# Performance work log

Measured on AMD Instinct MI355X. Metric: run time of the kernel, lower is better.

## Reference

```python
import jax, jax.numpy as jnp
import numpy as np

B = 16384
OBJ_FEAT = 1024
PVF_DIM = 1024
PPF_DIM = 64
HIDDEN = 512
OBJ_NUM = 1001        # param['object_num'] + 1
PRED_NUM = 132


def setup_inputs() -> dict:
    key = jax.random.key(0)
    ks = jax.random.split(key, 16)
    s = 0.02
    return {
        "inp_sf":  jax.random.normal(ks[0], (B, OBJ_FEAT), jnp.float32),
        "inp_of":  jax.random.normal(ks[1], (B, OBJ_FEAT), jnp.float32),
        "inp_ppf": jax.random.normal(ks[2], (B, PPF_DIM), jnp.float32),
        "inp_pvf": jax.random.normal(ks[3], (B, PVF_DIM), jnp.float32),
        "gt_s": jax.random.randint(ks[4], (B,), 0, OBJ_NUM, jnp.int32),
        "gt_o": jax.random.randint(ks[5], (B,), 0, OBJ_NUM, jnp.int32),
        # object_predictor: Linear(OBJ_FEAT, HIDDEN) -> Dropout -> ReLU -> Linear(HIDDEN, OBJ_NUM, bias=False)
        "W_obj1": jax.random.normal(ks[6], (OBJ_FEAT, HIDDEN), jnp.float32) * s,
        "b_obj1": jnp.zeros((HIDDEN,), jnp.float32),
        "W_obj2": jax.random.normal(ks[7], (HIDDEN, OBJ_NUM), jnp.float32) * s,
        # predicate_vis_feat_emb: Linear(PVF_DIM, HIDDEN) -> Dropout -> ReLU
        "W_pvf": jax.random.normal(ks[8], (PVF_DIM, HIDDEN), jnp.float32) * s,
        "b_pvf": jnp.zeros((HIDDEN,), jnp.float32),
        # predicate_feat_emb: Linear(HIDDEN + PPF_DIM, HIDDEN) -> ReLU
        "W_pf": jax.random.normal(ks[9], (HIDDEN + PPF_DIM, HIDDEN), jnp.float32) * s,
        "b_pf": jnp.zeros((HIDDEN,), jnp.float32),
        # predicate_predictor: Linear(HIDDEN, PRED_NUM, bias=False)
        "W_pred": jax.random.normal(ks[10], (HIDDEN, PRED_NUM), jnp.float32) * s,
        # knowledge table (frozen) + learnable scalar factor
        "so2p": jax.random.normal(ks[11], (OBJ_NUM * OBJ_NUM, PRED_NUM), jnp.float32) * s,
        "so2p_factor": jnp.zeros((1,), jnp.float32),
    }


def reference(inp_sf, inp_of, inp_ppf, inp_pvf, gt_s, gt_o,
              W_obj1, b_obj1, W_obj2, W_pvf, b_pvf, W_pf, b_pf, W_pred,
              so2p, so2p_factor):
    def obj_predictor(x):
        h = jnp.maximum(x @ W_obj1 + b_obj1, 0.0)  # Dropout is identity (p=0 / eval)
        return h @ W_obj2

    s_score = obj_predictor(inp_sf)               # [B, OBJ_NUM]
    o_score = obj_predictor(inp_of)               # [B, OBJ_NUM]

    pvf_emb = jnp.maximum(inp_pvf @ W_pvf + b_pvf, 0.0)                     # [B, HIDDEN]
    pf_emb = jnp.maximum(jnp.concatenate([pvf_emb, inp_ppf], axis=1) @ W_pf + b_pf, 0.0)
    p_score = pf_emb @ W_pred                     # [B, PRED_NUM]

    # one-hot(s) (x) one-hot(o) flattened then matmul with so2p == row gather at s*OBJ_NUM + o
    so_bias = so2p[gt_s * OBJ_NUM + gt_o]         # [B, PRED_NUM]
    so_bias = so_bias * jnp.exp(so2p_factor)      # use_knowledge=True

    return (s_score, o_score, p_score + so_bias)
```

## Files before the change

kernel.cpp:

```cpp
#include <hip/hip_runtime.h>
#include <hip/hip_bf16.h>
#include <cstdint>
#include <cstddef>

constexpr int BROWS   = 16384;
constexpr int OBJ_FEAT = 1024;
constexpr int PPF_DIM  = 64;
constexpr int HIDDEN   = 512;
constexpr int OBJ_NUM  = 1001;
constexpr int PRED_NUM = 132;
constexpr int OBJ_PAD  = 1024;
constexpr int PRED_PAD = 256;
constexpr int PF_K     = HIDDEN + PPF_DIM;

typedef __attribute__((ext_vector_type(8))) short bf16x8;
typedef __attribute__((ext_vector_type(4))) float f32x4;

static __device__ __forceinline__ unsigned short f2bf(float f) {
  unsigned int u = __float_as_uint(f);
  u += 0x7fffu + ((u >> 16) & 1u);
  return (unsigned short)(u >> 16);
}

__global__ void cast_w_all(const float* __restrict__ W0, const float* __restrict__ W1,
                           const float* __restrict__ W2, const float* __restrict__ W3,
                           const float* __restrict__ W4,
                           unsigned short* __restrict__ T0, unsigned short* __restrict__ T1,
                           unsigned short* __restrict__ T2, unsigned short* __restrict__ T3,
                           unsigned short* __restrict__ T4) {
  const int z = blockIdx.z;
  const float* W; unsigned short* T; int K, N, Npad;
  if      (z == 0) { W = W0; T = T0; K = 1024; N = 512;  Npad = 512;  }
  else if (z == 1) { W = W1; T = T1; K = 512;  N = 1001; Npad = 1024; }
  else if (z == 2) { W = W2; T = T2; K = 1024; N = 512;  Npad = 512;  }
  else if (z == 3) { W = W3; T = T3; K = 576;  N = 512;  Npad = 512;  }
  else             { W = W4; T = T4; K = 512;  N = 132;  Npad = 256;  }
  int n = blockIdx.y;
  int k = blockIdx.x * 256 + threadIdx.x;
  if (n >= Npad || k >= K) return;
  float v = (n < N) ? W[(size_t)k * N + n] : 0.0f;
  T[(size_t)n * K + k] = f2bf(v);
}

__global__ void cast_act(const float* __restrict__ sf, const float* __restrict__ of,
                         const float* __restrict__ pvf, const float* __restrict__ ppf,
                         unsigned short* __restrict__ Abf, unsigned short* __restrict__ Pvfb,
                         unsigned short* __restrict__ Ppfb) {
  const int z = blockIdx.z;
  const float* src; unsigned short* dst; size_t n4;
  if (z == 0)      { src = sf;  dst = Abf;                          n4 = (size_t)BROWS * OBJ_FEAT / 4; }
  else if (z == 1) { src = of;  dst = Abf + (size_t)BROWS * OBJ_FEAT; n4 = (size_t)BROWS * OBJ_FEAT / 4; }
  else if (z == 2) { src = pvf; dst = Pvfb;                         n4 = (size_t)BROWS * OBJ_FEAT / 4; }
  else             { src = ppf; dst = Ppfb;                         n4 = (size_t)BROWS * PPF_DIM / 4; }
  size_t stride = (size_t)gridDim.x * 256;
  for (size_t i = (size_t)blockIdx.x * 256 + threadIdx.x; i < n4; i += stride) {
    float4 v = reinterpret_cast<const float4*>(src)[i];
    ushort4 o;
    o.x = f2bf(v.x); o.y = f2bf(v.y); o.z = f2bf(v.z); o.w = f2bf(v.w);
    reinterpret_cast<ushort4*>(dst)[i] = o;
  }
}

template <int MODE>
__global__ __launch_bounds__(256)
void gemm_bf16(const unsigned short* __restrict__ A1, int ldA1, int K1,
               const unsigned short* __restrict__ A2, int ldA2,
               const unsigned short* __restrict__ Bt, int K,
               int Msplit,
               const unsigned short* __restrict__ A1b,
               const unsigned short* __restrict__ Btb,
               const float* __restrict__ biasb,
               float* __restrict__ outF, unsigned short* __restrict__ outB,
               int ldout, int Nreal,
               const float* __restrict__ bias,
               const int* __restrict__ gts, const int* __restrict__ gto,
               const float* __restrict__ so2p, const float* __restrict__ factor) {
  __shared__ unsigned short sA[128 * 32];
  __shared__ unsigned short sB[128 * 32];

  const int tid  = threadIdx.x;
  const int lane = tid & 63;
  const int wave = tid >> 6;
  const int wm   = wave >> 1;
  const int wn   = wave & 1;
  const int quad = lane >> 4;
  const int r16  = lane & 15;

  const int nwg = gridDim.x * gridDim.y;
  const int id  = blockIdx.y * gridDim.x + blockIdx.x;
  const int cpx = nwg >> 3;
  const int t   = (id & 7) * cpx + (id >> 3);
  const int m0  = (t / gridDim.x) * 128;
  const int n0  = (t % gridDim.x) * 128;

  const unsigned short* Abase = A1;
  const unsigned short* Bbase = Bt;
  const float* bias_p = bias;
  int mA = m0;
  if (m0 >= Msplit) { Abase = A1b; Bbase = Btb; bias_p = biasb; mA = m0 - Msplit; }

  f32x4 acc[4][4] = {};

  for (int k0 = 0; k0 < K; k0 += 32) {
    __syncthreads();
    const unsigned short* As; int lda, kk;
    if (k0 < K1) { As = Abase; lda = ldA1; kk = k0; }
    else         { As = A2;    lda = ldA2; kk = k0 - K1; }
#pragma unroll
    for (int j = 0; j < 2; ++j) {
      int ch = tid + j * 256, row = ch >> 2, c8 = ch & 3;
      const unsigned short* ga = As + (size_t)(mA + row) * lda + kk + c8 * 8;
      __builtin_amdgcn_global_load_lds(
          (const __attribute__((address_space(1))) void*)ga,
          (__attribute__((address_space(3))) void*)(sA + ch * 8), 16, 0, 0);
      const unsigned short* gb = Bbase + (size_t)(n0 + row) * K + k0 + c8 * 8;
      __builtin_amdgcn_global_load_lds(
          (const __attribute__((address_space(1))) void*)gb,
          (__attribute__((address_space(3))) void*)(sB + ch * 8), 16, 0, 0);
    }
    __syncthreads();

    bf16x8 af[4], bfr[4];
#pragma unroll
    for (int i = 0; i < 4; ++i)
      af[i] = *reinterpret_cast<const bf16x8*>(sA + (wm * 64 + i * 16 + r16) * 32 + quad * 8);
#pragma unroll
    for (int j = 0; j < 4; ++j)
      bfr[j] = *reinterpret_cast<const bf16x8*>(sB + (wn * 64 + j * 16 + r16) * 32 + quad * 8);
#pragma unroll
    for (int i = 0; i < 4; ++i)
#pragma unroll
      for (int j = 0; j < 4; ++j)
        acc[i][j] = __builtin_amdgcn_mfma_f32_16x16x32_bf16(af[i], bfr[j], acc[i][j], 0, 0, 0);
  }

  float ef = 0.0f;
  if (MODE == 2) ef = expf(factor[0]);

#pragma unroll
  for (int i = 0; i < 4; ++i) {
    int mbase = m0 + wm * 64 + i * 16 + quad * 4;
#pragma unroll
    for (int reg = 0; reg < 4; ++reg) {
      int m = mbase + reg;
      const float* so_row = nullptr;
      if (MODE == 2) {
        long rowidx = (long)gts[m] * OBJ_NUM + gto[m];
        so_row = so2p + rowidx * PRED_NUM;
      }
#pragma unroll
      for (int j = 0; j < 4; ++j) {
        int n = n0 + wn * 64 + j * 16 + r16;
        if (n < Nreal) {
          float v = acc[i][j][reg];
          if (MODE == 0) {
            v = fmaxf(v + bias_p[n], 0.0f);
            outB[(size_t)m * ldout + n] = f2bf(v);
          } else if (MODE == 1) {
            outF[(size_t)m * ldout + n] = v;
          } else {
            v += so_row[n] * ef;
            outF[(size_t)m * ldout + n] = v;
          }
        }
      }
    }
  }
}


extern "C" void kernel_launch(void* const* d_in, const int* in_sizes, int n_in,
                              void* d_out, int out_size, void* d_ws, size_t ws_size,
                              hipStream_t stream) {
  const float* inp_sf  = (const float*)d_in[0];
  const float* inp_of  = (const float*)d_in[1];
  const float* inp_ppf = (const float*)d_in[2];
  const float* inp_pvf = (const float*)d_in[3];
  const int*   gt_s    = (const int*)d_in[4];
  const int*   gt_o    = (const int*)d_in[5];
  const float* W_obj1  = (const float*)d_in[6];
  const float* b_obj1  = (const float*)d_in[7];
  const float* W_obj2  = (const float*)d_in[8];
  const float* W_pvf   = (const float*)d_in[9];
  const float* b_pvf   = (const float*)d_in[10];
  const float* W_pf    = (const float*)d_in[11];
  const float* b_pf    = (const float*)d_in[12];
  const float* W_pred  = (const float*)d_in[13];
  const float* so2p    = (const float*)d_in[14];
  const float* so2p_f  = (const float*)d_in[15];

  float* out_s = (float*)d_out;
  float* out_p = out_s + 2 * (size_t)BROWS * OBJ_NUM;

  char* ws = (char*)d_ws;
  unsigned short* H_buf = (unsigned short*)ws; ws += (size_t)3 * BROWS * HIDDEN * 2;
  unsigned short* Abf   = (unsigned short*)ws; ws += (size_t)2 * BROWS * OBJ_FEAT * 2;
  unsigned short* Pvfb  = (unsigned short*)ws; ws += (size_t)BROWS * OBJ_FEAT * 2;
  unsigned short* Ppfb  = (unsigned short*)ws; ws += (size_t)BROWS * PPF_DIM * 2;
  unsigned short* Wt_obj1 = (unsigned short*)ws; ws += (size_t)HIDDEN * OBJ_FEAT * 2;
  unsigned short* Wt_obj2 = (unsigned short*)ws; ws += (size_t)OBJ_PAD * HIDDEN * 2;
  unsigned short* Wt_pvf  = (unsigned short*)ws; ws += (size_t)HIDDEN * OBJ_FEAT * 2;
  unsigned short* Wt_pf   = (unsigned short*)ws; ws += (size_t)HIDDEN * PF_K * 2;
  unsigned short* Wt_pred = (unsigned short*)ws; ws += (size_t)PRED_PAD * HIDDEN * 2;
  unsigned short* H2 = Abf;

  cast_w_all<<<dim3(4, 1024, 5), 256, 0, stream>>>(
      W_obj1, W_obj2, W_pvf, W_pf, W_pred,
      Wt_obj1, Wt_obj2, Wt_pvf, Wt_pf, Wt_pred);
  cast_act<<<dim3(1024, 1, 4), 256, 0, stream>>>(
      inp_sf, inp_of, inp_pvf, inp_ppf, Abf, Pvfb, Ppfb);

  gemm_bf16<0><<<dim3(HIDDEN / 128, 3 * BROWS / 128), 256, 0, stream>>>(
      Abf, OBJ_FEAT, OBJ_FEAT, nullptr, 0,
      Wt_obj1, OBJ_FEAT,
      2 * BROWS, Pvfb, Wt_pvf, b_pvf,
      nullptr, H_buf, HIDDEN, HIDDEN, b_obj1,
      nullptr, nullptr, nullptr, nullptr);

  gemm_bf16<1><<<dim3(OBJ_PAD / 128, 2 * BROWS / 128), 256, 0, stream>>>(
      H_buf, HIDDEN, HIDDEN, nullptr, 0,
      Wt_obj2, HIDDEN,
      1 << 30, nullptr, nullptr, nullptr,
      out_s, nullptr, OBJ_NUM, OBJ_NUM, nullptr,
      nullptr, nullptr, nullptr, nullptr);

  gemm_bf16<0><<<dim3(HIDDEN / 128, BROWS / 128), 256, 0, stream>>>(
      H_buf + (size_t)2 * BROWS * HIDDEN, HIDDEN, HIDDEN, Ppfb, PPF_DIM,
      Wt_pf, PF_K,
      1 << 30, nullptr, nullptr, nullptr,
      nullptr, H2, HIDDEN, HIDDEN, b_pf,
      nullptr, nullptr, nullptr, nullptr);

  gemm_bf16<2><<<dim3(PRED_PAD / 128, BROWS / 128), 256, 0, stream>>>(
      H2, HIDDEN, HIDDEN, nullptr, 0,
      Wt_pred, HIDDEN,
      1 << 30, nullptr, nullptr, nullptr,
      out_p, nullptr, PRED_NUM, PRED_NUM, nullptr,
      gt_s, gt_o, so2p, so2p_f);

  (void)in_sizes; (void)n_in; (void)out_size; (void)ws_size;
}
```

Measured before the change: 1.000 ms.

## Fuse fp32-to-bf16 activation cast into GEMM A-tile loading

Removes the separate activation cast kernel and its bf16 staging buffers. The first-layer and predicate-feature GEMMs now read fp32 inputs directly into registers, prefetching the next K-slice after the barrier, then convert to bf16 and store to LDS. This avoids a full write and re-read of the bf16 activation copies. In exchange, the first GEMM loads twice the bytes per A tile through registers instead of using async global-to-LDS loads, and the LDS stores may hit more bank conflicts.

```diff
diff --git a/kernel.cpp b/kernel.cpp
--- a/kernel.cpp
+++ b/kernel.cpp
@@ -42,39 +42,20 @@
   T[(size_t)n * K + k] = f2bf(v);
 }
 
-__global__ void cast_act(const float* __restrict__ sf, const float* __restrict__ of,
-                         const float* __restrict__ pvf, const float* __restrict__ ppf,
-                         unsigned short* __restrict__ Abf, unsigned short* __restrict__ Pvfb,
-                         unsigned short* __restrict__ Ppfb) {
-  const int z = blockIdx.z;
-  const float* src; unsigned short* dst; size_t n4;
-  if (z == 0)      { src = sf;  dst = Abf;                          n4 = (size_t)BROWS * OBJ_FEAT / 4; }
-  else if (z == 1) { src = of;  dst = Abf + (size_t)BROWS * OBJ_FEAT; n4 = (size_t)BROWS * OBJ_FEAT / 4; }
-  else if (z == 2) { src = pvf; dst = Pvfb;                         n4 = (size_t)BROWS * OBJ_FEAT / 4; }
-  else             { src = ppf; dst = Ppfb;                         n4 = (size_t)BROWS * PPF_DIM / 4; }
-  size_t stride = (size_t)gridDim.x * 256;
-  for (size_t i = (size_t)blockIdx.x * 256 + threadIdx.x; i < n4; i += stride) {
-    float4 v = reinterpret_cast<const float4*>(src)[i];
-    ushort4 o;
-    o.x = f2bf(v.x); o.y = f2bf(v.y); o.z = f2bf(v.z); o.w = f2bf(v.w);
-    reinterpret_cast<ushort4*>(dst)[i] = o;
-  }
-}
-
-template <int MODE>
+template <int MODE, int FPA>
 __global__ __launch_bounds__(256)
-void gemm_bf16(const unsigned short* __restrict__ A1, int ldA1, int K1,
-               const unsigned short* __restrict__ A2, int ldA2,
-               const unsigned short* __restrict__ Bt, int K,
-               int Msplit,
-               const unsigned short* __restrict__ A1b,
-               const unsigned short* __restrict__ Btb,
-               const float* __restrict__ biasb,
-               float* __restrict__ outF, unsigned short* __restrict__ outB,
-               int ldout, int Nreal,
-               const float* __restrict__ bias,
-               const int* __restrict__ gts, const int* __restrict__ gto,
-               const float* __restrict__ so2p, const float* __restrict__ factor) {
+void gemm_fused(const unsigned short* __restrict__ A1, int ldA1, int K1,
+                const float* __restrict__ Af0, const float* __restrict__ Af1,
+                const float* __restrict__ Af2, int M1f, int ldAf,
+                const unsigned short* __restrict__ Bt, int K,
+                int Msplit,
+                const unsigned short* __restrict__ Btb,
+                const float* __restrict__ biasb,
+                float* __restrict__ outF, unsigned short* __restrict__ outB,
+                int ldout, int Nreal,
+                const float* __restrict__ bias,
+                const int* __restrict__ gts, const int* __restrict__ gto,
+                const float* __restrict__ so2p, const float* __restrict__ factor) {
   __shared__ unsigned short sA[128 * 32];
   __shared__ unsigned short sB[128 * 32];
 
@@ -93,32 +74,67 @@
   const int m0  = (t / gridDim.x) * 128;
   const int n0  = (t % gridDim.x) * 128;
 
-  const unsigned short* Abase = A1;
   const unsigned short* Bbase = Bt;
   const float* bias_p = bias;
-  int mA = m0;
-  if (m0 >= Msplit) { Abase = A1b; Bbase = Btb; bias_p = biasb; mA = m0 - Msplit; }
+  if (m0 >= Msplit) { Bbase = Btb; bias_p = biasb; }
+
+  const float* afb = nullptr;
+  if constexpr (FPA) {
+    if (m0 >= Msplit)    afb = Af2 + (size_t)(m0 - Msplit) * ldAf;
+    else if (m0 < M1f)   afb = Af0 + (size_t)m0 * ldAf;
+    else                 afb = Af1 + (size_t)(m0 - M1f) * ldAf;
+  }
+
+  float4 pa[4];
+  auto loadA = [&](int k0) {
+    const int kf = k0 - K1;
+#pragma unroll
+    for (int j = 0; j < 4; ++j) {
+      int ch = tid + j * 256, row = ch >> 3, c4 = (ch & 7) * 4;
+      pa[j] = *reinterpret_cast<const float4*>(afb + (size_t)row * ldAf + kf + c4);
+    }
+  };
+  if constexpr (FPA) {
+    if (K1 == 0) loadA(0);
+  }
 
   f32x4 acc[4][4] = {};
 
   for (int k0 = 0; k0 < K; k0 += 32) {
     __syncthreads();
-    const unsigned short* As; int lda, kk;
-    if (k0 < K1) { As = Abase; lda = ldA1; kk = k0; }
-    else         { As = A2;    lda = ldA2; kk = k0 - K1; }
+    if (!FPA || k0 < K1) {
+#pragma unroll
+      for (int j = 0; j < 2; ++j) {
+        int ch = tid + j * 256, row = ch >> 2, c8 = ch & 3;
+        const unsigned short* ga = A1 + (size_t)(m0 + row) * ldA1 + k0 + c8 * 8;
+        __builtin_amdgcn_global_load_lds(
+            (const __attribute__((address_space(1))) void*)ga,
+            (__attribute__((address_space(3))) void*)(sA + ch * 8), 16, 0, 0);
+      }
+    } else {
+#pragma unroll
+      for (int j = 0; j < 4; ++j) {
+        int ch = tid + j * 256, row = ch >> 3, c4 = (ch & 7) * 4;
+        ushort4 o;
+        o.x = f2bf(pa[j].x); o.y = f2bf(pa[j].y);
+        o.z = f2bf(pa[j].z); o.w = f2bf(pa[j].w);
+        *reinterpret_cast<ushort4*>(sA + row * 32 + c4) = o;
+      }
+    }
 #pragma unroll
     for (int j = 0; j < 2; ++j) {
       int ch = tid + j * 256, row = ch >> 2, c8 = ch & 3;
-      const unsigned short* ga = As + (size_t)(mA + row) * lda + kk + c8 * 8;
-      __builtin_amdgcn_global_load_lds(
-          (const __attribute__((address_space(1))) void*)ga,
-          (__attribute__((address_space(3))) void*)(sA + ch * 8), 16, 0, 0);
       const unsigned short* gb = Bbase + (size_t)(n0 + row) * K + k0 + c8 * 8;
       __builtin_amdgcn_global_load_lds(
           (const __attribute__((address_space(1))) void*)gb,
           (__attribute__((address_space(3))) void*)(sB + ch * 8), 16, 0, 0);
     }
     __syncthreads();
+
+    if constexpr (FPA) {
+      int kn = k0 + 32;
+      if (kn >= K1 && kn < K) loadA(kn);
+    }
 
     bf16x8 af[4], bfr[4];
 #pragma unroll
@@ -194,47 +210,46 @@
 
   char* ws = (char*)d_ws;
   unsigned short* H_buf = (unsigned short*)ws; ws += (size_t)3 * BROWS * HIDDEN * 2;
-  unsigned short* Abf   = (unsigned short*)ws; ws += (size_t)2 * BROWS * OBJ_FEAT * 2;
-  unsigned short* Pvfb  = (unsigned short*)ws; ws += (size_t)BROWS * OBJ_FEAT * 2;
-  unsigned short* Ppfb  = (unsigned short*)ws; ws += (size_t)BROWS * PPF_DIM * 2;
+  unsigned short* H2    = (unsigned short*)ws; ws += (size_t)BROWS * HIDDEN * 2;
   unsigned short* Wt_obj1 = (unsigned short*)ws; ws += (size_t)HIDDEN * OBJ_FEAT * 2;
   unsigned short* Wt_obj2 = (unsigned short*)ws; ws += (size_t)OBJ_PAD * HIDDEN * 2;
   unsigned short* Wt_pvf  = (unsigned short*)ws; ws += (size_t)HIDDEN * OBJ_FEAT * 2;
   unsigned short* Wt_pf   = (unsigned short*)ws; ws += (size_t)HIDDEN * PF_K * 2;
   unsigned short* Wt_pred = (unsigned short*)ws; ws += (size_t)PRED_PAD * HIDDEN * 2;
-  unsigned short* H2 = Abf;
 
   cast_w_all<<<dim3(4, 1024, 5), 256, 0, stream>>>(
       W_obj1, W_obj2, W_pvf, W_pf, W_pred,
       Wt_obj1, Wt_obj2, Wt_pvf, Wt_pf, Wt_pred);
-  cast_act<<<dim3(1024, 1, 4), 256, 0, stream>>>(
-      inp_sf, inp_of, inp_pvf, inp_ppf, Abf, Pvfb, Ppfb);
-
-  gemm_bf16<0><<<dim3(HIDDEN / 128, 3 * BROWS / 128), 256, 0, stream>>>(
-      Abf, OBJ_FEAT, OBJ_FEAT, nullptr, 0,
+
+  gemm_fused<0, 1><<<dim3(HIDDEN / 128, 3 * BROWS / 128), 256, 0, stream>>>(
+      nullptr, 0, 0,
+      inp_sf, inp_of, inp_pvf, BROWS, OBJ_FEAT,
       Wt_obj1, OBJ_FEAT,
-      2 * BROWS, Pvfb, Wt_pvf, b_pvf,
+      2 * BROWS, Wt_pvf, b_pvf,
       nullptr, H_buf, HIDDEN, HIDDEN, b_obj1,
       nullptr, nullptr, nullptr, nullptr);
 
-  gemm_bf16<1><<<dim3(OBJ_PAD / 128, 2 * BROWS / 128), 256, 0, stream>>>(
-      H_buf, HIDDEN, HIDDEN, nullptr, 0,
+  gemm_fused<1, 0><<<dim3(OBJ_PAD / 128, 2 * BROWS / 128), 256, 0, stream>>>(
+      H_buf, HIDDEN, HIDDEN,
+      nullptr, nullptr, nullptr, 0, 0,
       Wt_obj2, HIDDEN,
-      1 << 30, nullptr, nullptr, nullptr,
+      1 << 30, nullptr, nullptr,
       out_s, nullptr, OBJ_NUM, OBJ_NUM, nullptr,
       nullptr, nullptr, nullptr, nullptr);
 
-  gemm_bf16<0><<<dim3(HIDDEN / 128, BROWS / 128), 256, 0, stream>>>(
-      H_buf + (size_t)2 * BROWS * HIDDEN, HIDDEN, HIDDEN, Ppfb, PPF_DIM,
+  gemm_fused<0, 1><<<dim3(HIDDEN / 128, BROWS / 128), 256, 0, stream>>>(
+      H_buf + (size_t)2 * BROWS * HIDDEN, HIDDEN, HIDDEN,
+      inp_ppf, nullptr, nullptr, 1 << 30, PPF_DIM,
       Wt_pf, PF_K,
-      1 << 30, nullptr, nullptr, nullptr,
+      1 << 30, nullptr, nullptr,
       nullptr, H2, HIDDEN, HIDDEN, b_pf,
       nullptr, nullptr, nullptr, nullptr);
 
-  gemm_bf16<2><<<dim3(PRED_PAD / 128, BROWS / 128), 256, 0, stream>>>(
-      H2, HIDDEN, HIDDEN, nullptr, 0,
+  gemm_fused<2, 0><<<dim3(PRED_PAD / 128, BROWS / 128), 256, 0, stream>>>(
+      H2, HIDDEN, HIDDEN,
+      nullptr, nullptr, nullptr, 0, 0,
       Wt_pred, HIDDEN,
-      1 << 30, nullptr, nullptr, nullptr,
+      1 << 30, nullptr, nullptr,
       out_p, nullptr, PRED_NUM, PRED_NUM, nullptr,
       gt_s, gt_o, so2p, so2p_f);
 
```

Result: faster. 937.6 us (-6.3%).
